# Optimization experiments

Measured on AMD Instinct MI355X. Metric: run time of the kernel, lower is better.

Reference implementation:

```python
import jax, jax.numpy as jnp
import numpy as np

# Config constants (HNet300MConfig)
D = 1536          # d_model
H = 12            # n_heads // 2 used by chunk_attention
MAXC = 256        # max_chunks
MAXSEQ = 1024     # max_seq_length (size_embedding rows)
THRESH = 0.85     # boundary_threshold
B, S = 8, 1024


def setup_inputs() -> dict:
    key = jax.random.key(0)
    ks = jax.random.split(key, 10)
    def nrm(k, shape, scale=0.02):
        return jax.random.normal(k, shape, dtype=jnp.float32) * scale
    return {
        "x": jax.random.normal(ks[0], (B, S, D), dtype=jnp.float32),
        "boundaries": jax.random.uniform(ks[1], (B, S), dtype=jnp.float32),
        # nn.MultiheadAttention params
        "in_proj_w": nrm(ks[2], (3 * D, D)),
        "in_proj_b": jnp.zeros((3 * D,), jnp.float32),
        "out_w": nrm(ks[3], (D, D)),
        "out_b": jnp.zeros((D,), jnp.float32),
        # chunk_processor: Linear(D,2D) -> GELU -> Linear(2D,D) -> LayerNorm
        "w1": nrm(ks[4], (2 * D, D)),
        "b1": jnp.zeros((2 * D,), jnp.float32),
        "w2": nrm(ks[5], (D, 2 * D)),
        "b2": jnp.zeros((D,), jnp.float32),
        "ln_g": jnp.ones((D,), jnp.float32),
        "ln_b": jnp.zeros((D,), jnp.float32),
        "pos_enc": nrm(ks[6], (1, MAXC, D)),         # chunk_pos_encoding
        "size_emb": nrm(ks[7], (MAXSEQ, D), 1.0),    # size_embedding table
    }


def reference(x, boundaries, in_proj_w, in_proj_b, out_w, out_b,
              w1, b1, w2, b2, ln_g, ln_b, pos_enc, size_emb):
    dh = D // H
    # Chunk structure: boundary positions start chunks; seg_id = #boundaries up to
    # and including this token, minus 1. Tokens before the first boundary (seg=-1)
    # belong to no chunk. Final chunk runs from last boundary to seq end.
    is_b = boundaries > THRESH                                   # [B,S]
    seg = jnp.cumsum(is_b.astype(jnp.int32), axis=1) - 1         # [B,S]
    valid = seg >= 0

    # Per-chunk self-attention == full MHA with a block-diagonal mask.
    qkv = x @ in_proj_w.T + in_proj_b                            # [B,S,3D]
    q, k, v = jnp.split(qkv, 3, axis=-1)
    heads = lambda t: t.reshape(B, S, H, dh).transpose(0, 2, 1, 3)  # [B,H,S,dh]
    q, k, v = heads(q), heads(k), heads(v)
    scores = jnp.einsum('bhid,bhjd->bhij', q, k) / jnp.sqrt(jnp.float32(dh))
    blk = (seg[:, :, None] == seg[:, None, :]) & valid[:, :, None]  # [B,S,S]
    scores = jnp.where(blk[:, None], scores, jnp.float32(-1e9))
    attn = jax.nn.softmax(scores, axis=-1)
    ctx = jnp.einsum('bhij,bhjd->bhid', attn, v)
    ctx = ctx.transpose(0, 2, 1, 3).reshape(B, S, D)
    attn_out = ctx @ out_w.T + out_b                             # [B,S,D]

    # Ragged mean-pool per chunk (chunks beyond max_chunks are truncated;
    # tokens with seg=-1 or seg>=MAXC go to a dump bucket).
    seg_c = jnp.where(valid & (seg < MAXC), seg, MAXC)
    flat_seg = (seg_c + jnp.arange(B, dtype=jnp.int32)[:, None] * (MAXC + 1)).reshape(-1)
    sums = jax.ops.segment_sum(attn_out.reshape(-1, D), flat_seg,
                               num_segments=B * (MAXC + 1))
    cnts = jax.ops.segment_sum(jnp.ones((B * S,), jnp.float32), flat_seg,
                               num_segments=B * (MAXC + 1))
    sums = sums.reshape(B, MAXC + 1, D)[:, :MAXC]                # [B,MAXC,D]
    cnts = cnts.reshape(B, MAXC + 1)[:, :MAXC]                   # [B,MAXC]
    mean = sums / jnp.maximum(cnts, 1.0)[..., None]              # 0 for empty chunks

    # Size embedding added per non-empty chunk; empty (padding) chunks stay zero.
    lengths = cnts.astype(jnp.int32)
    size_idx = jnp.minimum(lengths, MAXSEQ - 1)
    size_vec = size_emb[size_idx] * (lengths > 0)[..., None].astype(jnp.float32)

    chunks = mean + size_vec + pos_enc                           # [B,MAXC,D]

    # chunk_processor (dropout inactive at inference)
    h = chunks @ w1.T + b1
    h = jax.nn.gelu(h, approximate=False)
    h = h @ w2.T + b2
    mu = jnp.mean(h, axis=-1, keepdims=True)
    var = jnp.mean((h - mu) ** 2, axis=-1, keepdims=True)
    out = (h - mu) / jnp.sqrt(var + 1e-5) * ln_g + ln_b
    return out
```

## Files before the change

kernel.cpp:

```cpp
#include <hip/hip_runtime.h>
#include <math.h>

#define NB 8
#define SEQ 1024
#define DM 1536
#define NHEAD 12
#define DHEAD 128
#define MAXC 256
#define QKVN 4608
#define THRESH 0.85f

typedef unsigned short u16;
typedef __attribute__((ext_vector_type(8))) __bf16 bf16x8;
typedef __attribute__((ext_vector_type(4))) float f32x4;

struct __align__(4) U2 { u16 x, y; };
struct __align__(8) U4 { u16 x, y, z, w; };

__device__ __forceinline__ float bf2f(u16 u) {
  union { unsigned i; float f; } c; c.i = ((unsigned)u) << 16; return c.f;
}
__device__ __forceinline__ u16 f2bf(float f) {
  union { float f; unsigned i; } c; c.f = f;
  unsigned r = c.i + 0x7FFFu + ((c.i >> 16) & 1u);
  return (u16)(r >> 16);
}

__global__ __launch_bounds__(256) void cvt5_bf16_kernel(
    const float* __restrict__ i0, u16* __restrict__ o0, int n0,
    const float* __restrict__ i1, u16* __restrict__ o1, int n1,
    const float* __restrict__ i2, u16* __restrict__ o2, int n2,
    const float* __restrict__ i3, u16* __restrict__ o3, int n3,
    const float* __restrict__ i4, u16* __restrict__ o4, int n4) {
  const int stride = gridDim.x * blockDim.x;
  const int t0 = blockIdx.x * blockDim.x + threadIdx.x;
  const float* ins[5] = {i0, i1, i2, i3, i4};
  u16* outs[5] = {o0, o1, o2, o3, o4};
  const int ns[5] = {n0, n1, n2, n3, n4};
#pragma unroll
  for (int a = 0; a < 5; ++a) {
    const float* in = ins[a];
    u16* out = outs[a];
    for (int i = t0; i < ns[a]; i += stride) {
      float4 f = ((const float4*)in)[i];
      U4 u; u.x = f2bf(f.x); u.y = f2bf(f.y); u.z = f2bf(f.z); u.w = f2bf(f.w);
      ((U4*)out)[i] = u;
    }
  }
}

__global__ __launch_bounds__(64) void segment_kernel(
    const float* __restrict__ bnd, int* __restrict__ nchunks,
    int* __restrict__ starts, int* __restrict__ lens) {
  const int b = blockIdx.x;
  const int lane = threadIdx.x;
  int running = 0;
  for (int g = 0; g < SEQ / 64; ++g) {
    int s = g * 64 + lane;
    bool isb = bnd[b * SEQ + s] > THRESH;
    unsigned long long mask = __ballot(isb ? 1 : 0);
    int excl = __popcll(mask & ((1ULL << lane) - 1ULL));
    if (isb) {
      int c = running + excl;
      if (c <= MAXC) starts[b * (MAXC + 1) + c] = s;
    }
    running += __popcll(mask);
  }
  if (lane == 0) nchunks[b] = running;
  __syncthreads();
  int ncl = min(running, MAXC);
  for (int c = lane; c < MAXC; c += 64) {
    int v = 0;
    if (c < ncl) {
      int st = starts[b * (MAXC + 1) + c];
      int en = (c + 1 < running) ? starts[b * (MAXC + 1) + c + 1] : SEQ;
      v = en - st;
    }
    lens[b * MAXC + c] = v;
  }
}

__global__ __launch_bounds__(512, 4) void gemmQKV_kernel(
    const u16* __restrict__ A, const u16* __restrict__ B,
    const int M, const int N, const int K,
    const float* __restrict__ bias, u16* __restrict__ outB) {
  __shared__ __align__(16) u16 lds[3][12288];
  const int tid = threadIdx.x;
  const int wid = tid >> 6;
  const int lane = tid & 63;
  const int cpx = gridDim.x >> 3;
  const int bid = ((int)blockIdx.x & 7) * cpx + ((int)blockIdx.x >> 3);
  const int MX = M >> 7;
  const int row0 = (bid % MX) << 7;
  const int col0 = (bid / MX) << 8;

  const int wr = wid >> 2;
  const int wc = wid & 3;
  const int rr = lane & 15;
  const int kg = lane >> 4;
  const int cw = rr * 4 + kg;
  const int slot = cw ^ ((cw >> 3) & 7);
  int srA, skA;
  { const int c = tid & 63; const int g = tid >> 6;
    const int gc = c ^ ((c >> 3) & 7);
    srA = g * 16 + (gc >> 2); skA = (gc & 3) * 8; }
  int srB[2], skB[2];
#pragma unroll
  for (int i = 0; i < 2; ++i) {
    const int s = i * 512 + tid;
    const int c = s & 63; const int g = s >> 6;
    const int gc = c ^ ((c >> 3) & 7);
    srB[i] = g * 16 + (gc >> 2); skB[i] = (gc & 3) * 8;
  }

  const int NT = K >> 5;

#define STAGE(t)                                                              \
  {                                                                           \
    const int _b = (t) % 3;                                                   \
    const int _kb = (t) << 5;                                                 \
    u16* ga = const_cast<u16*>(A) + (size_t)(row0 + srA) * K + _kb + skA;     \
    __builtin_amdgcn_global_load_lds(                                         \
        (__attribute__((address_space(1))) void*)ga,                          \
        (__attribute__((address_space(3))) void*)&lds[_b][(wid * 64) * 8],    \
        16, 0, 0);                                                            \
    _Pragma("unroll") for (int i = 0; i < 2; ++i) {                           \
      u16* gb = const_cast<u16*>(B) + (size_t)(col0 + srB[i]) * K + _kb +     \
                skB[i];                                                       \
      __builtin_amdgcn_global_load_lds(                                       \
          (__attribute__((address_space(1))) void*)gb,                        \
          (__attribute__((address_space(3))) void*)&lds[_b]                   \
              [4096 + (i * 512 + wid * 64) * 8], 16, 0, 0);                   \
    }                                                                         \
  }

  f32x4 acc[4][4] = {};

  STAGE(0); STAGE(1);
  asm volatile("s_waitcnt vmcnt(3)" ::: "memory");
  __builtin_amdgcn_s_barrier();

  for (int t = 0; t < NT; ++t) {
    const int buf = t % 3;
    bf16x8 bf[4], af[4];
#pragma unroll
    for (int n = 0; n < 4; ++n)
      bf[n] = *(const bf16x8*)&lds[buf][4096 + ((wc * 4 + n) * 64 + slot) * 8];
#pragma unroll
    for (int m = 0; m < 4; ++m)
      af[m] = *(const bf16x8*)&lds[buf][((wr * 4 + m) * 64 + slot) * 8];
    if (t + 2 < NT) STAGE(t + 2);
    __builtin_amdgcn_s_setprio(1);
#pragma unroll
    for (int m = 0; m < 4; ++m)
#pragma unroll
      for (int n = 0; n < 4; ++n)
        acc[m][n] = __builtin_amdgcn_mfma_f32_16x16x32_bf16(af[m], bf[n], acc[m][n], 0, 0, 0);
    __builtin_amdgcn_s_setprio(0);
    if (t + 2 < NT) {
      asm volatile("s_waitcnt vmcnt(3)" ::: "memory");
    } else if (t + 1 < NT) {
      asm volatile("s_waitcnt vmcnt(0)" ::: "memory");
    }
    __builtin_amdgcn_s_barrier();
  }
#undef STAGE

#pragma unroll
  for (int m = 0; m < 4; ++m) {
#pragma unroll
    for (int n = 0; n < 4; ++n) {
      const int col = col0 + wc * 64 + n * 16 + rr;
      const float bs = bias[col];
#pragma unroll
      for (int j = 0; j < 4; ++j) {
        const int row = row0 + wr * 64 + m * 16 + (lane >> 4) * 4 + j;
        outB[(size_t)row * N + col] = f2bf(acc[m][n][j] + bs);
      }
    }
  }
}

template <int MODE>
__global__ __launch_bounds__(256, 4) void gemm_bf16_kernel(
    const u16* __restrict__ A, const u16* __restrict__ B,
    const int M, const int N, const int K,
    const float* __restrict__ bias,
    u16* __restrict__ outB, float* __restrict__ outF,
    const int* __restrict__ lens, const float* __restrict__ semb,
    const float* __restrict__ pos) {
  __shared__ __align__(16) u16 As[3][128 * 32];
  __shared__ __align__(16) u16 Bs[3][64 * 32];
  const int tid = threadIdx.x;
  const int wave = tid >> 6;
  const int lane = tid & 63;
  const int row0 = blockIdx.y * 128;
  const int col0 = blockIdx.x * 64;
  const int wm = (wave >> 1) * 64;
  const int wn = (wave & 1) * 32;
  const int gch = lane ^ ((lane >> 3) & 7);
  const int sr = gch >> 2;
  const int sc = (gch & 3) * 8;
  const int rr = lane & 15;
  const int kg = lane >> 4;
  const int cwant = rr * 4 + kg;
  const int slot = cwant ^ ((cwant >> 3) & 7);
  const int NT = K >> 5;
  f32x4 acc[4][2] = {};

#define STAGE64(t)                                                            \
  {                                                                           \
    const int _b = (t) % 3;                                                   \
    const int _k = (t) << 5;                                                  \
    _Pragma("unroll") for (int tt = 0; tt < 2; ++tt) {                        \
      const int li = wave * 2 + tt;                                           \
      u16* ga = const_cast<u16*>(A) + (size_t)(row0 + li * 16 + sr) * K +     \
                _k + sc;                                                      \
      __builtin_amdgcn_global_load_lds(                                       \
          (__attribute__((address_space(1))) void*)ga,                        \
          (__attribute__((address_space(3))) void*)(As[_b] + li * 512), 16,   \
          0, 0);                                                              \
    }                                                                         \
    u16* gb = const_cast<u16*>(B) + (size_t)(col0 + wave * 16 + sr) * K +     \
              _k + sc;                                                        \
    __builtin_amdgcn_global_load_lds(                                         \
        (__attribute__((address_space(1))) void*)gb,                          \
        (__attribute__((address_space(3))) void*)(Bs[_b] + wave * 512), 16,   \
        0, 0);                                                                \
  }

  STAGE64(0); STAGE64(1);
  asm volatile("s_waitcnt vmcnt(3)" ::: "memory");
  __builtin_amdgcn_s_barrier();

  for (int t = 0; t < NT; ++t) {
    const int cb = t % 3;
    bf16x8 bfr[2], af[4];
#pragma unroll
    for (int n = 0; n < 2; ++n)
      bfr[n] = *(const bf16x8*)(Bs[cb] + ((wn >> 4) + n) * 512 + slot * 8);
#pragma unroll
    for (int m = 0; m < 4; ++m)
      af[m] = *(const bf16x8*)(As[cb] + ((wm >> 4) + m) * 512 + slot * 8);
    if (t + 2 < NT) STAGE64(t + 2);
#pragma unroll
    for (int m = 0; m < 4; ++m)
#pragma unroll
      for (int n = 0; n < 2; ++n)
        acc[m][n] = __builtin_amdgcn_mfma_f32_16x16x32_bf16(af[m], bfr[n], acc[m][n], 0, 0, 0);
    if (t + 2 < NT) {
      asm volatile("s_waitcnt vmcnt(3)" ::: "memory");
    } else if (t + 1 < NT) {
      asm volatile("s_waitcnt vmcnt(0)" ::: "memory");
    }
    __builtin_amdgcn_s_barrier();
  }
#undef STAGE64

  const int rg = (lane >> 4) * 4;
#pragma unroll
  for (int m = 0; m < 4; ++m) {
#pragma unroll
    for (int n = 0; n < 2; ++n) {
      const int col = col0 + wn + n * 16 + rr;
#pragma unroll
      for (int j = 0; j < 4; ++j) {
        const int row = row0 + wm + m * 16 + rg + j;
        float v = acc[m][n][j];
        if (MODE == 2) {
          const int len = lens[row];
          float val = 0.f;
          if (len > 0) {
            const int si = len < 1023 ? len : 1023;
            val = v + bias[col] + semb[(size_t)si * DM + col];
          }
          val += pos[(size_t)(row & (MAXC - 1)) * DM + col];
          outB[(size_t)row * N + col] = f2bf(val);
        } else if (MODE == 3) {
          float z = v + bias[col];
          float gel = 0.5f * z * (1.f + erff(z * 0.70710678118654752440f));
          outB[(size_t)row * N + col] = f2bf(gel);
        } else {
          outF[(size_t)row * N + col] = v + bias[col];
        }
      }
    }
  }
}

__global__ __launch_bounds__(64) void chunk_attn_kernel(
    const u16* __restrict__ qkv, const int* __restrict__ nchunks,
    const int* __restrict__ starts, const int* __restrict__ lens,
    u16* __restrict__ pooled) {
  __shared__ float g_lds[SEQ];
  const int h = blockIdx.x;
  const int c = blockIdx.y;
  const int b = blockIdx.z;
  const int lane = threadIdx.x;
  const int nc = min(nchunks[b], MAXC);
  u16* prow = pooled + ((size_t)(b * MAXC + c)) * DM + h * DHEAD;
  if (c >= nc) {
    U2 z; z.x = 0; z.y = 0;
    *(U2*)(prow + lane * 2) = z;
    return;
  }
  const int s0 = starts[b * (MAXC + 1) + c];
  const int L = lens[b * MAXC + c];
  const u16* Qb = qkv + ((size_t)(b * SEQ + s0)) * QKVN + h * DHEAD;
  const u16* Kb = Qb + DM;
  const u16* Vb = Qb + 2 * DM;

  const int col = lane & 15;
  const int grp = lane >> 4;
  const float scale = 0.08838834764831845f;
  const int half = lane >> 5;
  const int dl4 = (lane & 31) * 4;

  float a[4] = {0.f, 0.f, 0.f, 0.f};

  if (L <= 16) {
    const int rc = col < L ? col : (L - 1);
    bf16x8 qf[4], kf[4];
#pragma unroll
    for (int s = 0; s < 4; ++s) {
      qf[s] = *(const bf16x8*)(Qb + (size_t)rc * QKVN + s * 32 + grp * 8);
      kf[s] = *(const bf16x8*)(Kb + (size_t)rc * QKVN + s * 32 + grp * 8);
    }
    f32x4 sc = {0.f, 0.f, 0.f, 0.f};
#pragma unroll
    for (int s = 0; s < 4; ++s)
      sc = __builtin_amdgcn_mfma_f32_16x16x32_bf16(qf[s], kf[s], sc, 0, 0, 0);
    const bool kvalid = col < L;
    float g = 0.f;
#pragma unroll
    for (int j = 0; j < 4; ++j) {
      float sj = sc[j] * scale;
      float mv = kvalid ? sj : -3e38f;
      mv = fmaxf(mv, __shfl_xor(mv, 1));
      mv = fmaxf(mv, __shfl_xor(mv, 2));
      mv = fmaxf(mv, __shfl_xor(mv, 4));
      mv = fmaxf(mv, __shfl_xor(mv, 8));
      float pv = kvalid ? __expf(sj - mv) : 0.f;
      float dv = pv;
      dv += __shfl_xor(dv, 1);
      dv += __shfl_xor(dv, 2);
      dv += __shfl_xor(dv, 4);
      dv += __shfl_xor(dv, 8);
      const bool rv = (grp * 4 + j) < L;
      g += rv ? pv / dv : 0.f;
    }
    g += __shfl_xor(g, 16);
    g += __shfl_xor(g, 32);
    float gv[8];
#pragma unroll
    for (int i = 0; i < 8; ++i) {
      const int jj = 2 * i + half;
      float gb = __shfl(g, jj < 16 ? jj : 0);
      gv[i] = (jj < L) ? gb : 0.f;
    }
#pragma unroll
    for (int i = 0; i < 8; ++i) {
      const int jj = 2 * i + half;
      const int jc = jj < L ? jj : (L - 1);
      if (2 * i < L) {
        U4 vv = *(const U4*)(Vb + (size_t)jc * QKVN + dl4);
        a[0] += gv[i] * bf2f(vv.x); a[1] += gv[i] * bf2f(vv.y);
        a[2] += gv[i] * bf2f(vv.z); a[3] += gv[i] * bf2f(vv.w);
      }
    }
  } else {
    float* gw = g_lds;
    for (int j = lane; j < L; j += 64) gw[j] = 0.f;
    const int NT = (L + 15) >> 4;
    for (int qt = 0; qt < NT; ++qt) {
      const int qr = qt * 16 + col;
      const int qrc = qr < L ? qr : (L - 1);
      bf16x8 qf[4];
#pragma unroll
      for (int s = 0; s < 4; ++s)
        qf[s] = *(const bf16x8*)(Qb + (size_t)qrc * QKVN + s * 32 + grp * 8);

      float m[4] = {-3e38f, -3e38f, -3e38f, -3e38f};
      float den[4] = {0.f, 0.f, 0.f, 0.f};
      for (int kt = 0; kt < NT; ++kt) {
        const int kr = kt * 16 + col;
        const bool kvalid = kr < L;
        const int krc = kvalid ? kr : (L - 1);
        f32x4 sc = {0.f, 0.f, 0.f, 0.f};
#pragma unroll
        for (int s = 0; s < 4; ++s) {
          bf16x8 kf = *(const bf16x8*)(Kb + (size_t)krc * QKVN + s * 32 + grp * 8);
          sc = __builtin_amdgcn_mfma_f32_16x16x32_bf16(qf[s], kf, sc, 0, 0, 0);
        }
#pragma unroll
        for (int j = 0; j < 4; ++j) {
          float sj = sc[j] * scale;
          float mv = kvalid ? sj : -3e38f;
          mv = fmaxf(mv, __shfl_xor(mv, 1));
          mv = fmaxf(mv, __shfl_xor(mv, 2));
          mv = fmaxf(mv, __shfl_xor(mv, 4));
          mv = fmaxf(mv, __shfl_xor(mv, 8));
          float mn = fmaxf(m[j], mv);
          float pv = kvalid ? __expf(sj - mn) : 0.f;
          pv += __shfl_xor(pv, 1);
          pv += __shfl_xor(pv, 2);
          pv += __shfl_xor(pv, 4);
          pv += __shfl_xor(pv, 8);
          den[j] = den[j] * __expf(m[j] - mn) + pv;
          m[j] = mn;
        }
      }
      float inv[4];
#pragma unroll
      for (int j = 0; j < 4; ++j) {
        const bool rv = (qt * 16 + grp * 4 + j) < L;
        inv[j] = rv ? 1.f / den[j] : 0.f;
      }
      for (int kt = 0; kt < NT; ++kt) {
        const int kr = kt * 16 + col;
        const bool kvalid = kr < L;
        const int krc = kvalid ? kr : (L - 1);
        f32x4 sc = {0.f, 0.f, 0.f, 0.f};
#pragma unroll
        for (int s = 0; s < 4; ++s) {
          bf16x8 kf = *(const bf16x8*)(Kb + (size_t)krc * QKVN + s * 32 + grp * 8);
          sc = __builtin_amdgcn_mfma_f32_16x16x32_bf16(qf[s], kf, sc, 0, 0, 0);
        }
        float colsum = 0.f;
#pragma unroll
        for (int j = 0; j < 4; ++j)
          colsum += __expf(sc[j] * scale - m[j]) * inv[j];
        colsum += __shfl_xor(colsum, 16);
        colsum += __shfl_xor(colsum, 32);
        if (grp == 0 && kvalid) gw[kt * 16 + col] += colsum;
      }
    }
    for (int j = 0; j < L; j += 2) {
      const int jj = j + half;
      const bool jv = jj < L;
      float gj = jv ? gw[jj] : 0.f;
      const int jc = jv ? jj : 0;
      U4 vv = *(const U4*)(Vb + (size_t)jc * QKVN + dl4);
      a[0] += gj * bf2f(vv.x); a[1] += gj * bf2f(vv.y);
      a[2] += gj * bf2f(vv.z); a[3] += gj * bf2f(vv.w);
    }
  }
  const float invL = 1.f / (float)L;
#pragma unroll
  for (int i = 0; i < 4; ++i) {
    a[i] += __shfl_xor(a[i], 32);
    a[i] *= invL;
  }
  if (lane < 32) {
    U4 r; r.x = f2bf(a[0]); r.y = f2bf(a[1]); r.z = f2bf(a[2]); r.w = f2bf(a[3]);
    *(U4*)(prow + dl4) = r;
  }
}

__global__ __launch_bounds__(256) void ln_kernel(
    const float* __restrict__ h2, const float* __restrict__ gamma,
    const float* __restrict__ beta, float* __restrict__ out) {
  const int row = blockIdx.x;
  const float* x = h2 + (size_t)row * DM;
  float* o = out + (size_t)row * DM;
  const int tid = threadIdx.x;
  float v[6];
  float s = 0.f;
#pragma unroll
  for (int i = 0; i < 6; ++i) { v[i] = x[tid + i * 256]; s += v[i]; }
  __shared__ float red[8];
#pragma unroll
  for (int off = 32; off; off >>= 1) s += __shfl_xor(s, off);
  if ((tid & 63) == 0) red[tid >> 6] = s;
  __syncthreads();
  const float mu = (red[0] + red[1] + red[2] + red[3]) * (1.f / (float)DM);
  float vs = 0.f;
#pragma unroll
  for (int i = 0; i < 6; ++i) { float d = v[i] - mu; vs += d * d; }
#pragma unroll
  for (int off = 32; off; off >>= 1) vs += __shfl_xor(vs, off);
  __shared__ float red2[8];
  if ((tid & 63) == 0) red2[tid >> 6] = vs;
  __syncthreads();
  const float var = (red2[0] + red2[1] + red2[2] + red2[3]) * (1.f / (float)DM);
  const float inv = rsqrtf(var + 1e-5f);
#pragma unroll
  for (int i = 0; i < 6; ++i) {
    const int cidx = tid + i * 256;
    o[cidx] = (v[i] - mu) * inv * gamma[cidx] + beta[cidx];
  }
}

extern "C" void kernel_launch(void* const* d_in, const int* in_sizes, int n_in,
                              void* d_out, int out_size, void* d_ws, size_t ws_size,
                              hipStream_t stream) {
  const float* x    = (const float*)d_in[0];
  const float* bnd  = (const float*)d_in[1];
  const float* wqkv = (const float*)d_in[2];
  const float* bqkv = (const float*)d_in[3];
  const float* wout = (const float*)d_in[4];
  const float* bout = (const float*)d_in[5];
  const float* w1   = (const float*)d_in[6];
  const float* b1   = (const float*)d_in[7];
  const float* w2   = (const float*)d_in[8];
  const float* b2   = (const float*)d_in[9];
  const float* lng  = (const float*)d_in[10];
  const float* lnb  = (const float*)d_in[11];
  const float* pos  = (const float*)d_in[12];
  const float* semb = (const float*)d_in[13];
  float* out = (float*)d_out;

  char* ws = (char*)d_ws;
  size_t off = 0;
  auto alloc = [&](size_t bytes) -> char* {
    char* p = ws + off;
    off += (bytes + 255) & ~(size_t)255;
    return p;
  };
  u16* x_bf    = (u16*)alloc((size_t)NB * SEQ * DM * 2);
  u16* wqkv_bf = (u16*)alloc((size_t)3 * DM * DM * 2);
  u16* wout_bf = (u16*)alloc((size_t)DM * DM * 2);
  u16* w1_bf   = (u16*)alloc((size_t)2 * DM * DM * 2);
  u16* w2_bf   = (u16*)alloc((size_t)2 * DM * DM * 2);
  u16* qkv_bf  = (u16*)alloc((size_t)NB * SEQ * QKVN * 2);
  int* nchunks = (int*)alloc(NB * 4);
  int* starts  = (int*)alloc(NB * (MAXC + 1) * 4);
  int* lens    = (int*)alloc(NB * MAXC * 4);
  u16* pooled  = (u16*)alloc((size_t)NB * MAXC * DM * 2);
  u16* chunks  = (u16*)alloc((size_t)NB * MAXC * DM * 2);
  u16* h1      = (u16*)alloc((size_t)NB * MAXC * 2 * DM * 2);
  float* h2    = (float*)alloc((size_t)NB * MAXC * DM * 4);
  (void)ws_size; (void)in_sizes; (void)n_in; (void)out_size;

  cvt5_bf16_kernel<<<2048, 256, 0, stream>>>(
      x, x_bf, NB * SEQ * DM / 4,
      wqkv, wqkv_bf, 3 * DM * DM / 4,
      wout, wout_bf, DM * DM / 4,
      w1, w1_bf, 2 * DM * DM / 4,
      w2, w2_bf, 2 * DM * DM / 4);

  segment_kernel<<<NB, 64, 0, stream>>>(bnd, nchunks, starts, lens);

  gemmQKV_kernel<<<(NB * SEQ / 128) * (QKVN / 256), 512, 0, stream>>>(
      x_bf, wqkv_bf, NB * SEQ, QKVN, DM, bqkv, qkv_bf);

  chunk_attn_kernel<<<dim3(NHEAD, MAXC, NB), 64, 0, stream>>>(
      qkv_bf, nchunks, starts, lens, pooled);

  gemm_bf16_kernel<2><<<dim3(DM / 64, NB * MAXC / 128), 256, 0, stream>>>(
      pooled, wout_bf, NB * MAXC, DM, DM, bout, chunks, nullptr, lens, semb, pos);

  gemm_bf16_kernel<3><<<dim3(2 * DM / 64, NB * MAXC / 128), 256, 0, stream>>>(
      chunks, w1_bf, NB * MAXC, 2 * DM, DM, b1, h1, nullptr, nullptr, nullptr, nullptr);

  gemm_bf16_kernel<4><<<dim3(DM / 64, NB * MAXC / 128), 256, 0, stream>>>(
      h1, w2_bf, NB * MAXC, DM, 2 * DM, b2, nullptr, h2, nullptr, nullptr, nullptr);

  ln_kernel<<<NB * MAXC, 256, 0, stream>>>(h2, lng, lnb, out);
}
```

Before: 322.6 us.

## Double K-tile depth in QKV GEMM and split stage loads into two phases

The QKV GEMM now processes 64 K elements per pipeline step instead of 32, doubling the LDS footprint of each of the three buffers. Each step is split into two half-phases: each issues part of the next-next tile's global-to-LDS loads, separated by barriers around the MFMA blocks. Launch bounds drop to one block per SM minimum. The intent is fewer loop iterations and barriers per unit of work and better interleaving of memory issue with MFMA, at the cost of more LDS (lower occupancy) and extra barriers inside each step.

```diff
diff --git a/kernel.cpp b/kernel.cpp
--- a/kernel.cpp
+++ b/kernel.cpp
@@ -80,11 +80,11 @@
   }
 }
 
-__global__ __launch_bounds__(512, 4) void gemmQKV_kernel(
+__global__ __launch_bounds__(512, 1) void gemmQKV_kernel(
     const u16* __restrict__ A, const u16* __restrict__ B,
     const int M, const int N, const int K,
     const float* __restrict__ bias, u16* __restrict__ outB) {
-  __shared__ __align__(16) u16 lds[3][12288];
+  __shared__ __align__(16) u16 lds[3][24576];
   const int tid = threadIdx.x;
   const int wid = tid >> 6;
   const int lane = tid & 63;
@@ -100,71 +100,111 @@
   const int kg = lane >> 4;
   const int cw = rr * 4 + kg;
   const int slot = cw ^ ((cw >> 3) & 7);
-  int srA, skA;
+  int rA, kA;
   { const int c = tid & 63; const int g = tid >> 6;
     const int gc = c ^ ((c >> 3) & 7);
-    srA = g * 16 + (gc >> 2); skA = (gc & 3) * 8; }
-  int srB[2], skB[2];
-#pragma unroll
-  for (int i = 0; i < 2; ++i) {
-    const int s = i * 512 + tid;
+    rA = g * 16 + (gc >> 2); kA = (gc & 3) * 8; }
+  int rB[2], kB[2];
+#pragma unroll
+  for (int j = 0; j < 2; ++j) {
+    const int s = j * 512 + tid;
     const int c = s & 63; const int g = s >> 6;
     const int gc = c ^ ((c >> 3) & 7);
-    srB[i] = g * 16 + (gc >> 2); skB[i] = (gc & 3) * 8;
-  }
-
-  const int NT = K >> 5;
-
-#define STAGE(t)                                                              \
+    rB[j] = g * 16 + (gc >> 2); kB[j] = (gc & 3) * 8;
+  }
+
+  const int NT = K >> 6;
+
+#define STAGE_P0(t)                                                           \
   {                                                                           \
     const int _b = (t) % 3;                                                   \
-    const int _kb = (t) << 5;                                                 \
-    u16* ga = const_cast<u16*>(A) + (size_t)(row0 + srA) * K + _kb + skA;     \
+    const int _kb = (t) << 6;                                                 \
+    _Pragma("unroll") for (int kh = 0; kh < 2; ++kh) {                        \
+      u16* ga = const_cast<u16*>(A) + (size_t)(row0 + rA) * K + _kb +         \
+                kh * 32 + kA;                                                 \
+      __builtin_amdgcn_global_load_lds(                                       \
+          (__attribute__((address_space(1))) void*)ga,                        \
+          (__attribute__((address_space(3))) void*)&lds[_b]                   \
+              [kh * 4096 + tid * 8], 16, 0, 0);                               \
+    }                                                                         \
+    u16* gb = const_cast<u16*>(B) + (size_t)(col0 + rB[0]) * K + _kb +        \
+              kB[0];                                                          \
     __builtin_amdgcn_global_load_lds(                                         \
-        (__attribute__((address_space(1))) void*)ga,                          \
-        (__attribute__((address_space(3))) void*)&lds[_b][(wid * 64) * 8],    \
+        (__attribute__((address_space(1))) void*)gb,                          \
+        (__attribute__((address_space(3))) void*)&lds[_b][8192 + tid * 8],    \
         16, 0, 0);                                                            \
-    _Pragma("unroll") for (int i = 0; i < 2; ++i) {                           \
-      u16* gb = const_cast<u16*>(B) + (size_t)(col0 + srB[i]) * K + _kb +     \
-                skB[i];                                                       \
+  }
+#define STAGE_P1(t)                                                           \
+  {                                                                           \
+    const int _b = (t) % 3;                                                   \
+    const int _kb = (t) << 6;                                                 \
+    u16* gb1 = const_cast<u16*>(B) + (size_t)(col0 + rB[1]) * K + _kb +       \
+               kB[1];                                                         \
+    __builtin_amdgcn_global_load_lds(                                         \
+        (__attribute__((address_space(1))) void*)gb1,                         \
+        (__attribute__((address_space(3))) void*)&lds[_b]                     \
+            [8192 + 4096 + tid * 8], 16, 0, 0);                               \
+    _Pragma("unroll") for (int j = 0; j < 2; ++j) {                           \
+      u16* gb = const_cast<u16*>(B) + (size_t)(col0 + rB[j]) * K + _kb +      \
+                32 + kB[j];                                                   \
       __builtin_amdgcn_global_load_lds(                                       \
           (__attribute__((address_space(1))) void*)gb,                        \
           (__attribute__((address_space(3))) void*)&lds[_b]                   \
-              [4096 + (i * 512 + wid * 64) * 8], 16, 0, 0);                   \
+              [8192 + 8192 + j * 4096 + tid * 8], 16, 0, 0);                  \
     }                                                                         \
   }
 
   f32x4 acc[4][4] = {};
 
-  STAGE(0); STAGE(1);
-  asm volatile("s_waitcnt vmcnt(3)" ::: "memory");
+  STAGE_P0(0); STAGE_P1(0);
+  STAGE_P0(1); STAGE_P1(1);
+  asm volatile("s_waitcnt vmcnt(6)" ::: "memory");
   __builtin_amdgcn_s_barrier();
 
   for (int t = 0; t < NT; ++t) {
     const int buf = t % 3;
-    bf16x8 bf[4], af[4];
+    bf16x8 b0[4], a0[4];
 #pragma unroll
     for (int n = 0; n < 4; ++n)
-      bf[n] = *(const bf16x8*)&lds[buf][4096 + ((wc * 4 + n) * 64 + slot) * 8];
+      b0[n] = *(const bf16x8*)&lds[buf][8192 + ((wc * 4 + n) * 64 + slot) * 8];
 #pragma unroll
     for (int m = 0; m < 4; ++m)
-      af[m] = *(const bf16x8*)&lds[buf][((wr * 4 + m) * 64 + slot) * 8];
-    if (t + 2 < NT) STAGE(t + 2);
+      a0[m] = *(const bf16x8*)&lds[buf][((wr * 4 + m) * 64 + slot) * 8];
+    if (t + 2 < NT) STAGE_P0(t + 2);
+    __builtin_amdgcn_s_barrier();
     __builtin_amdgcn_s_setprio(1);
 #pragma unroll
     for (int m = 0; m < 4; ++m)
 #pragma unroll
       for (int n = 0; n < 4; ++n)
-        acc[m][n] = __builtin_amdgcn_mfma_f32_16x16x32_bf16(af[m], bf[n], acc[m][n], 0, 0, 0);
+        acc[m][n] = __builtin_amdgcn_mfma_f32_16x16x32_bf16(a0[m], b0[n], acc[m][n], 0, 0, 0);
+    __builtin_amdgcn_s_setprio(0);
+    __builtin_amdgcn_s_barrier();
+    bf16x8 b1[4], a1[4];
+#pragma unroll
+    for (int n = 0; n < 4; ++n)
+      b1[n] = *(const bf16x8*)&lds[buf][8192 + 8192 + ((wc * 4 + n) * 64 + slot) * 8];
+#pragma unroll
+    for (int m = 0; m < 4; ++m)
+      a1[m] = *(const bf16x8*)&lds[buf][4096 + ((wr * 4 + m) * 64 + slot) * 8];
+    if (t + 2 < NT) STAGE_P1(t + 2);
+    __builtin_amdgcn_s_barrier();
+    __builtin_amdgcn_s_setprio(1);
+#pragma unroll
+    for (int m = 0; m < 4; ++m)
+#pragma unroll
+      for (int n = 0; n < 4; ++n)
+        acc[m][n] = __builtin_amdgcn_mfma_f32_16x16x32_bf16(a1[m], b1[n], acc[m][n], 0, 0, 0);
     __builtin_amdgcn_s_setprio(0);
     if (t + 2 < NT) {
-      asm volatile("s_waitcnt vmcnt(3)" ::: "memory");
+      asm volatile("s_waitcnt vmcnt(6)" ::: "memory");
     } else if (t + 1 < NT) {
       asm volatile("s_waitcnt vmcnt(0)" ::: "memory");
     }
     __builtin_amdgcn_s_barrier();
   }
-#undef STAGE
+#undef STAGE_P0
+#undef STAGE_P1
 
 #pragma unroll
   for (int m = 0; m < 4; ++m) {
```

After: 336.2 us. 4.2% more time.
